# Kernel tuning notes

Hardware: AMD Instinct MI355X
Metric: run time of the kernel (lower is better)

## Reference

```python
import jax, jax.numpy as jnp
import numpy as np

# Hyperparameters from init_kwargs
MIN_STREAK_HIGH = 4
MIN_STREAK_LOW = 7
MIN_STREAKS_HIGH_ACT = 2
MIN_STREAKS_LOW_ACT = 3
HIGH_IMPACT_INIT = 0.18
LOW_IMPACT_INIT = 0.05
MAX_ADJUST = 0.35
HIGH_DECAY = 0.5
LOW_DECAY = 0.5

B, T = 16384, 4096


def setup_inputs() -> dict:
    key = jax.random.key(0)
    k1, k2 = jax.random.split(key)
    drowsiness_index = jax.random.uniform(k1, (B, 1), dtype=jnp.float32)
    gesture_sequence = jax.random.randint(k2, (B, T, 1), 0, 3, dtype=jnp.int32)
    return {"drowsiness_index": drowsiness_index, "gesture_sequence": gesture_sequence}


def _adjustments(gesture_sequence):
    # [B, T] yawning mask (gesture class 2)
    m = jnp.squeeze(gesture_sequence, axis=-1) == 2
    Tn = m.shape[1]
    r = jnp.arange(Tn, dtype=jnp.int32)  # [T]
    # Vectorized run-length encoding: index of most recent non-yawning frame.
    # reset[b, t] = t where m==False, else -1; running max gives last reset position.
    reset = jnp.where(m, jnp.int32(-1), r[None, :])  # [B, T]
    last_reset = jax.lax.cummax(reset, axis=1)  # [B, T]
    cnt = jnp.where(m, r[None, :] - last_reset, 0)  # streak length so far at t
    # A streak ends at t if m[t] and (t is last or m[t+1] is False).
    next_m = jnp.concatenate([m[:, 1:], jnp.zeros((m.shape[0], 1), dtype=bool)], axis=1)
    is_end = m & ~next_m  # [B, T]
    high_count = jnp.sum(is_end & (cnt >= MIN_STREAK_HIGH), axis=1)  # [B] int32
    low_count = jnp.sum(is_end & (cnt >= MIN_STREAK_LOW), axis=1)
    high_adj = HIGH_IMPACT_INIT * jnp.exp(
        -HIGH_DECAY * (high_count - MIN_STREAKS_HIGH_ACT).astype(jnp.float32))
    high_adj = jnp.where(high_count >= MIN_STREAKS_HIGH_ACT, high_adj, 0.0)
    low_adj = LOW_IMPACT_INIT * jnp.exp(
        -LOW_DECAY * (low_count - MIN_STREAKS_LOW_ACT).astype(jnp.float32))
    low_adj = jnp.where(low_count >= MIN_STREAKS_LOW_ACT, low_adj, 0.0)
    total = jnp.minimum(high_adj + low_adj, MAX_ADJUST)  # [B]
    return total[:, None]  # [B, 1]


def reference(drowsiness_index, gesture_sequence):
    adj = _adjustments(gesture_sequence)
    return jnp.clip(drowsiness_index + adj, 0.0, 1.0)
```

## Files before the change

kernel.cpp:

```cpp
#include <hip/hip_runtime.h>
#include <stdint.h>


#define NROWS 16384
#define TLEN  4096

__global__ __launch_bounds__(256, 4) void yawn_adjust_kernel(
    const float* __restrict__ drows,
    const int* __restrict__ gest,
    float* __restrict__ out)
{
    const int lane = threadIdx.x & 63;
    const int row  = blockIdx.x * 4 + (threadIdx.x >> 6);
    if (row >= NROWS) return;

    const int* gp = gest + (size_t)row * TLEN + lane;

    uint32_t mlo = 0u, mhi = 0u;
    #pragma unroll
    for (int j0 = 0; j0 < 64; j0 += 16) {
        int v[16];
        #pragma unroll
        for (int k = 0; k < 16; ++k)
            v[k] = gp[(j0 + k) * 64];
        #pragma unroll
        for (int k = 0; k < 16; ++k) {
            unsigned long long b = __ballot(v[k] == 2);
            if (lane == j0 + k) {
                mlo = (uint32_t)b;
                mhi = (uint32_t)(b >> 32);
            }
        }
    }

    uint64_t m  = ((uint64_t)mhi << 32) | (uint64_t)mlo;
    bool     full = (m == ~0ull);
    uint64_t nm = ~m;
    int lead  = full ? 64 : (int)__builtin_ctzll(nm);
    int trail = full ? 64 : (int)__builtin_clzll(nm);

    int leadc  = full ? 0 : lead;
    int trailc = full ? 0 : trail;
    uint64_t mi = full ? 0ull : m;
    mi = (mi >> leadc) << leadc;
    mi = (mi << trailc) >> trailc;

    uint64_t w = mi & (mi >> 1);
    w &= (w >> 2);
    int ch = __builtin_popcountll(w & ~(w << 1));
    uint64_t w7 = w & (w >> 3);
    int cl = __builtin_popcountll(w7 & ~(w7 << 1));

    #pragma unroll
    for (int off = 1, len = 64; off < 64; off <<= 1, len <<= 1) {
        int bch    = __shfl_down(ch,    (unsigned)off, 64);
        int bcl    = __shfl_down(cl,    (unsigned)off, 64);
        int blead  = __shfl_down(lead,  (unsigned)off, 64);
        int btrail = __shfl_down(trail, (unsigned)off, 64);

        bool afull = (lead  == len);
        bool bfull = (blead == len);
        int junction = trail + blead;
        bool interior = (!afull) && (!bfull);
        ch += bch + ((interior && junction >= 4) ? 1 : 0);
        cl += bcl + ((interior && junction >= 7) ? 1 : 0);
        lead  = afull ? (len + blead)  : lead;
        trail = bfull ? (len + trail)  : btrail;
    }

    if (lane == 0) {
        int hc, lc;
        if (lead == TLEN) {
            hc = 1; lc = 1;
        } else {
            hc = ch + (lead >= 4 ? 1 : 0) + (trail >= 4 ? 1 : 0);
            lc = cl + (lead >= 7 ? 1 : 0) + (trail >= 7 ? 1 : 0);
        }
        float hadj = (hc >= 2) ? 0.18f * expf(-0.5f * (float)(hc - 2)) : 0.0f;
        float ladj = (lc >= 3) ? 0.05f * expf(-0.5f * (float)(lc - 3)) : 0.0f;
        float tot  = fminf(hadj + ladj, 0.35f);
        float r    = drows[row] + tot;
        out[row]   = fminf(fmaxf(r, 0.0f), 1.0f);
    }
}

extern "C" void kernel_launch(void* const* d_in, const int* in_sizes, int n_in,
                              void* d_out, int out_size, void* d_ws, size_t ws_size,
                              hipStream_t stream) {
    (void)in_sizes; (void)n_in; (void)d_ws; (void)ws_size; (void)out_size;
    const float* drows = (const float*)d_in[0];
    const int*   gest  = (const int*)d_in[1];
    float*       out   = (float*)d_out;
    dim3 grid(NROWS / 4);
    yawn_adjust_kernel<<<grid, 256, 0, stream>>>(drows, gest, out);
}
```

Measured before the change: 354.4 us.

## Load gestures as int4 and run streak logic on four interleaved bitmasks

Each lane now loads int4 vectors, so one wavefront reads 1024 contiguous ints per load instead of 64. The 256-frame chunk per lane is kept as four interleaved 64-bit masks, and streak counting, lead and trail runs are computed with cross-mask shifts. The shuffle reduction then covers only 16 lanes, each holding a 256-frame segment. The aim is fewer, wider global loads per byte. The cost is more complex bit logic with a higher chance of subtle edge-case errors.

```diff
diff --git a/kernel.cpp b/kernel.cpp
--- a/kernel.cpp
+++ b/kernel.cpp
@@ -7,52 +7,69 @@
 
 __global__ __launch_bounds__(256, 4) void yawn_adjust_kernel(
     const float* __restrict__ drows,
-    const int* __restrict__ gest,
+    const int4* __restrict__ gest4,
     float* __restrict__ out)
 {
     const int lane = threadIdx.x & 63;
     const int row  = blockIdx.x * 4 + (threadIdx.x >> 6);
-    if (row >= NROWS) return;
 
-    const int* gp = gest + (size_t)row * TLEN + lane;
+    const int4* gp = gest4 + (size_t)row * (TLEN / 4) + lane;
 
-    uint32_t mlo = 0u, mhi = 0u;
+    uint64_t m0 = 0, m1 = 0, m2 = 0, m3 = 0;
     #pragma unroll
-    for (int j0 = 0; j0 < 64; j0 += 16) {
-        int v[16];
+    for (int g = 0; g < 2; ++g) {
+        int4 v[8];
         #pragma unroll
-        for (int k = 0; k < 16; ++k)
-            v[k] = gp[(j0 + k) * 64];
+        for (int k = 0; k < 8; ++k)
+            v[k] = gp[(g * 8 + k) * 64];
         #pragma unroll
-        for (int k = 0; k < 16; ++k) {
-            unsigned long long b = __ballot(v[k] == 2);
-            if (lane == j0 + k) {
-                mlo = (uint32_t)b;
-                mhi = (uint32_t)(b >> 32);
-            }
+        for (int k = 0; k < 8; ++k) {
+            const int j = g * 8 + k;
+            uint64_t b0 = __ballot(v[k].x == 2);
+            uint64_t b1 = __ballot(v[k].y == 2);
+            uint64_t b2 = __ballot(v[k].z == 2);
+            uint64_t b3 = __ballot(v[k].w == 2);
+            if (lane == j) { m0 = b0; m1 = b1; m2 = b2; m3 = b3; }
         }
     }
 
-    uint64_t m  = ((uint64_t)mhi << 32) | (uint64_t)mlo;
-    bool     full = (m == ~0ull);
-    uint64_t nm = ~m;
-    int lead  = full ? 64 : (int)__builtin_ctzll(nm);
-    int trail = full ? 64 : (int)__builtin_clzll(nm);
+    uint64_t allw = m0 & m1 & m2 & m3;
+    bool full = (allw == ~0ull);
+    uint64_t z  = ~allw;
+    uint64_t zs = full ? 1ull : z;
+    int iF = __builtin_ctzll(zs);
+    int iL = 63 - __builtin_clzll(zs);
+    int cF = ((~m0 >> iF) & 1) ? 0 : ((~m1 >> iF) & 1) ? 1 : ((~m2 >> iF) & 1) ? 2 : 3;
+    int cL = ((~m3 >> iL) & 1) ? 3 : ((~m2 >> iL) & 1) ? 2 : ((~m1 >> iL) & 1) ? 1 : 0;
+    int lead  = full ? 256 : (4 * iF + cF);
+    int ez    = 4 * iL + cL;
+    int trail = full ? 256 : (255 - ez);
 
-    int leadc  = full ? 0 : lead;
-    int trailc = full ? 0 : trail;
-    uint64_t mi = full ? 0ull : m;
-    mi = (mi >> leadc) << leadc;
-    mi = (mi << trailc) >> trailc;
+    uint64_t lowbits  = (1ull << iF) - 1;
+    uint64_t lowF     = 1ull << iF;
+    uint64_t highbits = ~((2ull << iL) - 1);
+    uint64_t highF    = 1ull << iL;
+    uint64_t i0 = full ? 0ull : (m0 & ~(lowbits | ((0 < cF) ? lowF : 0) | highbits | ((0 > cL) ? highF : 0)));
+    uint64_t i1 = full ? 0ull : (m1 & ~(lowbits | ((1 < cF) ? lowF : 0) | highbits | ((1 > cL) ? highF : 0)));
+    uint64_t i2 = full ? 0ull : (m2 & ~(lowbits | ((2 < cF) ? lowF : 0) | highbits | ((2 > cL) ? highF : 0)));
+    uint64_t i3 = full ? 0ull : (m3 & ~(lowbits | ((3 < cF) ? lowF : 0) | highbits | ((3 > cL) ? highF : 0)));
 
-    uint64_t w = mi & (mi >> 1);
-    w &= (w >> 2);
-    int ch = __builtin_popcountll(w & ~(w << 1));
-    uint64_t w7 = w & (w >> 3);
-    int cl = __builtin_popcountll(w7 & ~(w7 << 1));
+    uint64_t h0 = i0 >> 1, h1 = i1 >> 1, h2 = i2 >> 1;
+    uint64_t w0 = i0 & i1 & i2 & i3;
+    uint64_t w1 = i1 & i2 & i3 & h0;
+    uint64_t w2 = i2 & i3 & h0 & h1;
+    uint64_t w3 = i3 & h0 & h1 & h2;
+    uint64_t u0 = w0 & w3;
+    uint64_t u1 = w1 & (w0 >> 1);
+    uint64_t u2 = w2 & (w1 >> 1);
+    uint64_t u3 = w3 & (w2 >> 1);
+    int ch = __builtin_popcountll(w0 & ~(w3 << 1)) + __builtin_popcountll(w1 & ~w0)
+           + __builtin_popcountll(w2 & ~w1)        + __builtin_popcountll(w3 & ~w2);
+    int cl = __builtin_popcountll(u0 & ~(u3 << 1)) + __builtin_popcountll(u1 & ~u0)
+           + __builtin_popcountll(u2 & ~u1)        + __builtin_popcountll(u3 & ~u2);
 
     #pragma unroll
-    for (int off = 1, len = 64; off < 64; off <<= 1, len <<= 1) {
+    for (int off = 1, len = 256; off < 16; off <<= 1, len <<= 1) {
         int bch    = __shfl_down(ch,    (unsigned)off, 64);
         int bcl    = __shfl_down(cl,    (unsigned)off, 64);
         int blead  = __shfl_down(lead,  (unsigned)off, 64);
@@ -64,8 +81,8 @@
         bool interior = (!afull) && (!bfull);
         ch += bch + ((interior && junction >= 4) ? 1 : 0);
         cl += bcl + ((interior && junction >= 7) ? 1 : 0);
-        lead  = afull ? (len + blead)  : lead;
-        trail = bfull ? (len + trail)  : btrail;
+        lead  = afull ? (len + blead) : lead;
+        trail = bfull ? (len + trail) : btrail;
     }
 
     if (lane == 0) {
@@ -89,8 +106,8 @@
                               hipStream_t stream) {
     (void)in_sizes; (void)n_in; (void)d_ws; (void)ws_size; (void)out_size;
     const float* drows = (const float*)d_in[0];
-    const int*   gest  = (const int*)d_in[1];
+    const int4*  gest4 = (const int4*)d_in[1];
     float*       out   = (float*)d_out;
     dim3 grid(NROWS / 4);
-    yawn_adjust_kernel<<<grid, 256, 0, stream>>>(drows, gest, out);
+    yawn_adjust_kernel<<<grid, 256, 0, stream>>>(drows, gest4, out);
 }
```

After: 355.0 us. About the same (+0.1%).
